# Kernel optimization log

Hardware: AMD Instinct MI355X
Metric: run time of the kernel (lower is better)

Reference implementation:

```python
import jax, jax.numpy as jnp
import numpy as np

N = 50000      # nodes
E = 800000     # edges (avg degree 16)
IN = 128       # in_feats
H = 4          # num_heads
D = 32         # out_feats per head
EF = 32        # edge_feats
NT = 4         # num node types
ET = 8         # num edge types
NEG_SLOPE = 0.2


def setup_inputs() -> dict:
    key = jax.random.key(0)
    ks = jax.random.split(key, 12)
    feat = jax.random.normal(ks[0], (N, IN), dtype=jnp.float32)
    src = jax.random.randint(ks[1], (E,), 0, N, dtype=jnp.int32)
    dst = jax.random.randint(ks[2], (E,), 0, N, dtype=jnp.int32)
    etype = jax.random.randint(ks[3], (E,), 0, ET, dtype=jnp.int32)
    ntype = jax.random.randint(ks[4], (N,), 0, NT, dtype=jnp.int32)
    # learned parameters (xavier-ish scale)
    W_fc = jax.random.normal(ks[5], (H * D, IN), dtype=jnp.float32) * (2.0 / (IN + H * D)) ** 0.5
    W_e = jax.random.normal(ks[6], (H * EF, EF), dtype=jnp.float32) * (2.0 / (EF + H * EF)) ** 0.5
    edge_emb = jax.random.normal(ks[7], (ET, EF), dtype=jnp.float32) * 0.1
    attn_l = jax.random.normal(ks[8], (NT, H, D), dtype=jnp.float32) * 0.1
    attn_r = jax.random.normal(ks[9], (NT, H, D), dtype=jnp.float32) * 0.1
    attn_e = jax.random.normal(ks[10], (ET, H, EF), dtype=jnp.float32) * 0.1
    return dict(feat=feat, W_fc=W_fc, W_e=W_e, edge_emb=edge_emb,
                attn_l=attn_l, attn_r=attn_r, attn_e=attn_e,
                src=src, dst=dst, etype=etype, ntype=ntype)


def reference(feat, W_fc, W_e, edge_emb, attn_l, attn_r, attn_e, src, dst, etype, ntype):
    n = feat.shape[0]
    # node projection: (N, IN) @ (IN, H*D) -> (N, H, D)
    feat_src = (feat @ W_fc.T).reshape(n, H, D)

    # edge-type embedding: original multiplies the etype id (as float) by edge_emb[etype]
    embed_e = etype.astype(feat.dtype)[:, None] * edge_emb[etype]          # (E, EF)
    embed_e = (embed_e @ W_e.T).reshape(-1, H, EF)                          # (E, H, EF)
    ee = jnp.einsum('ehf,ehf->eh', embed_e, attn_e[etype])                  # (E, H)

    # per-node-type attention scores
    el = jnp.einsum('nhd,nhd->nh', feat_src, attn_l[ntype])                 # (N, H)
    er = jnp.einsum('nhd,nhd->nh', feat_src, attn_r[ntype])                 # (N, H)

    e = el[src] + er[dst] + ee                                              # (E, H)
    e = jnp.where(e > 0, e, NEG_SLOPE * e)                                  # leaky relu

    # edge softmax over incoming edges of each destination node
    m = jax.ops.segment_max(e, dst, num_segments=n)                         # (N, H)
    m = jnp.where(jnp.isfinite(m), m, 0.0)                                  # guard empty segments
    ex = jnp.exp(e - m[dst])
    den = jax.ops.segment_sum(ex, dst, num_segments=n)                      # (N, H)
    a = ex / den[dst]                                                       # (E, H)

    # aggregate: rst[v] = sum_{(u->v)} a * feat_src[u]
    msgs = feat_src[src] * a[:, :, None]                                    # (E, H, D)
    rst = jax.ops.segment_sum(msgs, dst, num_segments=n)                    # (N, H, D)
    return rst, a[:, :, None]
```

## Files before the change

kernel.cpp:

```cpp
#include <hip/hip_runtime.h>
#include <hip/hip_bf16.h>

#define NEG_SLOPE 0.2f

typedef __attribute__((ext_vector_type(4))) float f32x4;
typedef __attribute__((ext_vector_type(8))) short s16x8;

__device__ __forceinline__ short f2bf(float x) {
    __hip_bfloat16 h = __float2bfloat16(x);
    return *reinterpret_cast<short*>(&h);
}

#define PCHUNK 64
__global__ __launch_bounds__(256) void k_proj(const float* __restrict__ feat,
                                              const float* __restrict__ Wfc,
                                              __hip_bfloat16* __restrict__ fsrcb,
                                              const float* __restrict__ attn_l,
                                              const float* __restrict__ attn_r,
                                              const int* __restrict__ ntype,
                                              float* __restrict__ el,
                                              float* __restrict__ er, int n) {
    __shared__ short Wb[128 * 128];
    __shared__ float s_al[512], s_ar[512];
    const int t = threadIdx.x;
    for (int idx = t; idx < 128 * 128; idx += 256) {
        int c = idx >> 7, k = idx & 127;
        Wb[c * 128 + ((((k >> 3) ^ (c & 7)) << 3) | (k & 7))] = f2bf(Wfc[idx]);
    }
    s_al[t] = attn_l[t]; s_al[t + 256] = attn_l[t + 256];
    s_ar[t] = attn_r[t]; s_ar[t + 256] = attn_r[t + 256];
    __syncthreads();

    const int w   = t >> 6;
    const int l   = t & 63;
    const int c16 = l & 15;
    const int g0  = l >> 4;
    const int nchunks = (n + PCHUNK - 1) / PCHUNK;

    for (int chunk = blockIdx.x; chunk < nchunks; chunk += gridDim.x) {
        const int rbase = chunk * PCHUNK + w * 16;
        const float* ap = feat + (size_t)min(rbase + c16, n - 1) * 128;
        s16x8 av[4];
        #pragma unroll
        for (int kq = 0; kq < 4; ++kq) {
            float4 q0 = *(const float4*)(ap + g0 * 8 + kq * 32);
            float4 q1 = *(const float4*)(ap + g0 * 8 + kq * 32 + 4);
            s16x8 a;
            a[0] = f2bf(q0.x); a[1] = f2bf(q0.y); a[2] = f2bf(q0.z); a[3] = f2bf(q0.w);
            a[4] = f2bf(q1.x); a[5] = f2bf(q1.y); a[6] = f2bf(q1.z); a[7] = f2bf(q1.w);
            av[kq] = a;
        }
        f32x4 acc[8];
        #pragma unroll
        for (int f = 0; f < 8; ++f) acc[f] = (f32x4)0.f;
        #pragma unroll
        for (int kq = 0; kq < 4; ++kq) {
            const int g = g0 + kq * 4;
            #pragma unroll
            for (int f = 0; f < 8; ++f) {
                const int c = f * 16 + c16;
                const s16x8 bv = *(const s16x8*)&Wb[c * 128 + ((g ^ (c & 7)) << 3)];
                acc[f] = __builtin_amdgcn_mfma_f32_16x16x32_bf16(av[kq], bv, acc[f], 0, 0, 0);
            }
        }
        #pragma unroll
        for (int reg = 0; reg < 4; ++reg) {
            const int rr = rbase + g0 * 4 + reg;
            const bool ok = rr < n;
            if (ok) {
                #pragma unroll
                for (int f = 0; f < 8; ++f)
                    fsrcb[(size_t)rr * 128 + f * 16 + c16] = __float2bfloat16(acc[f][reg]);
            }
            const int nt = ntype[min(rr, n - 1)];
            const float* alp = s_al + nt * 128;
            const float* arp = s_ar + nt * 128;
            float pe[4], pr[4];
            #pragma unroll
            for (int h = 0; h < 4; ++h) {
                float d0 = acc[2 * h][reg], d1 = acc[2 * h + 1][reg];
                pe[h] = d0 * alp[h * 32 + c16] + d1 * alp[h * 32 + 16 + c16];
                pr[h] = d0 * arp[h * 32 + c16] + d1 * arp[h * 32 + 16 + c16];
            }
            #pragma unroll
            for (int msk = 1; msk < 16; msk <<= 1) {
                #pragma unroll
                for (int h = 0; h < 4; ++h) {
                    pe[h] += __shfl_xor(pe[h], msk, 64);
                    pr[h] += __shfl_xor(pr[h], msk, 64);
                }
            }
            if (c16 == 0 && ok) {
                float4 e4; e4.x = pe[0]; e4.y = pe[1]; e4.z = pe[2]; e4.w = pe[3];
                float4 r4; r4.x = pr[0]; r4.y = pr[1]; r4.z = pr[2]; r4.w = pr[3];
                *(float4*)(el + (size_t)rr * 4) = e4;
                *(float4*)(er + (size_t)rr * 4) = r4;
            }
        }
    }
}

__global__ void k_ee(const float* __restrict__ W_e, const float* __restrict__ edge_emb,
                     const float* __restrict__ attn_e, float* __restrict__ eet) {
    int t = threadIdx.x;
    if (t >= 8 * 4) return;
    int et = t >> 2, h = t & 3;
    float ee = 0.f;
    for (int f = 0; f < 32; ++f) {
        float acc = 0.f;
        for (int g = 0; g < 32; ++g)
            acc += W_e[((size_t)h * 32 + f) * 32 + g] * edge_emb[et * 32 + g];
        ee += acc * attn_e[((size_t)et * 4 + h) * 32 + f];
    }
    eet[t] = ee * (float)et;
}

__global__ void k_deg(const int* __restrict__ dst, int* __restrict__ deg, int ne) {
    int e = blockIdx.x * blockDim.x + threadIdx.x;
    if (e < ne) atomicAdd(deg + dst[e], 1);
}

#define SC_ELEMS 1024
__global__ __launch_bounds__(256) void k_scan_sum(const int* __restrict__ deg,
                                                  int* __restrict__ bsum, int n) {
    __shared__ int red[256];
    const int t = threadIdx.x;
    const int base = blockIdx.x * SC_ELEMS;
    int s = 0;
    #pragma unroll
    for (int i = 0; i < 4; ++i) {
        int idx = base + t * 4 + i;
        if (idx < n) s += deg[idx];
    }
    red[t] = s;
    __syncthreads();
    for (int off = 128; off > 0; off >>= 1) {
        if (t < off) red[t] += red[t + off];
        __syncthreads();
    }
    if (t == 0) bsum[blockIdx.x] = red[0];
}

__global__ __launch_bounds__(1024) void k_scan_mid(int* __restrict__ bsum, int nb) {
    __shared__ int sh[1024];
    const int t = threadIdx.x;
    int v = (t < nb) ? bsum[t] : 0;
    sh[t] = v;
    __syncthreads();
    for (int off = 1; off < 1024; off <<= 1) {
        int add = (t >= off) ? sh[t - off] : 0;
        __syncthreads();
        sh[t] += add;
        __syncthreads();
    }
    if (t < nb) bsum[t] = sh[t] - v;
}

__global__ __launch_bounds__(256) void k_scan_out(const int* __restrict__ deg,
                                                  const int* __restrict__ bsum,
                                                  int* __restrict__ offs,
                                                  int* __restrict__ cursor, int n) {
    __shared__ int sh[256];
    const int t = threadIdx.x;
    const int base = blockIdx.x * SC_ELEMS + t * 4;
    int v[4], s = 0;
    #pragma unroll
    for (int i = 0; i < 4; ++i) {
        int idx = base + i;
        v[i] = (idx < n) ? deg[idx] : 0;
        s += v[i];
    }
    sh[t] = s;
    __syncthreads();
    const int mine = s;
    for (int off = 1; off < 256; off <<= 1) {
        int add = (t >= off) ? sh[t - off] : 0;
        __syncthreads();
        sh[t] += add;
        __syncthreads();
    }
    int run = bsum[blockIdx.x] + sh[t] - mine;
    #pragma unroll
    for (int i = 0; i < 4; ++i) {
        int idx = base + i;
        if (idx < n) { offs[idx] = run; cursor[idx] = run; run += v[i]; }
    }
    if (blockIdx.x == gridDim.x - 1 && t == 255) offs[n] = run;
}

__global__ void k_edge(const int* __restrict__ src, const int* __restrict__ dst,
                       const int* __restrict__ etype, const float* __restrict__ el,
                       const float* __restrict__ er, const float* __restrict__ eet,
                       int* __restrict__ cursor, float* __restrict__ pay, int ne) {
    int e = blockIdx.x * blockDim.x + threadIdx.x;
    if (e >= ne) return;
    int s = src[e], d = dst[e], et = etype[e];
    float4 l = *(const float4*)(el + (size_t)s * 4);
    float4 r = *(const float4*)(er + (size_t)d * 4);
    float4 te = *(const float4*)(eet + (size_t)et * 4);
    float4 v;
    v.x = l.x + r.x + te.x;
    v.y = l.y + r.y + te.y;
    v.z = l.z + r.z + te.z;
    v.w = l.w + r.w + te.w;
    v.x = v.x > 0.f ? v.x : NEG_SLOPE * v.x;
    v.y = v.y > 0.f ? v.y : NEG_SLOPE * v.y;
    v.z = v.z > 0.f ? v.z : NEG_SLOPE * v.z;
    v.w = v.w > 0.f ? v.w : NEG_SLOPE * v.w;
    int pos = atomicAdd(cursor + d, 1);
    *(float4*)(pay + (size_t)pos * 8) = v;
    int2 es; es.x = e; es.y = s;
    *(int2*)(pay + (size_t)pos * 8 + 4) = es;
}

#define CHUNK 128
__global__ __launch_bounds__(128) void k_aggfull(const int* __restrict__ offs,
                                                 const float* __restrict__ pay,
                                                 const __hip_bfloat16* __restrict__ fsrcb,
                                                 float* __restrict__ aBuf,
                                                 float* __restrict__ rst) {
    __shared__ int   s_src[CHUNK];
    __shared__ int   s_eid[CHUNK];
    __shared__ float s_sc[4][CHUNK];
    __shared__ float s_p[4][CHUNK];
    __shared__ float s_mr[8];
    const int d = blockIdx.x;
    const int j = threadIdx.x;
    const int h = j >> 5;
    const int b = offs[d], e1 = offs[d + 1];
    const int deg = e1 - b;

    float m = -1e30f, den = 0.f, acc = 0.f;
    for (int c0 = 0; c0 < deg; c0 += CHUNK) {
        const int cn = min(CHUNK, deg - c0);
        if (j < cn) {
            const float* p8 = pay + (size_t)(b + c0 + j) * 8;
            float4 v = *(const float4*)p8;
            int2 es = *(const int2*)(p8 + 4);
            s_sc[0][j] = v.x; s_sc[1][j] = v.y; s_sc[2][j] = v.z; s_sc[3][j] = v.w;
            s_eid[j] = es.x; s_src[j] = es.y;
        }
        __syncthreads();
        float mc = -1e30f;
        for (int k = j & 31; k < cn; k += 32) mc = fmaxf(mc, s_sc[h][k]);
        #pragma unroll
        for (int w = 1; w < 32; w <<= 1) mc = fmaxf(mc, __shfl_xor(mc, w, 64));
        mc = fmaxf(mc, m);
        float scale = __expf(m - mc);
        den *= scale; acc *= scale; m = mc;
        if ((j & 31) == 0) s_mr[h] = m;
        __syncthreads();
        if (j < cn) {
            s_p[0][j] = __expf(s_sc[0][j] - s_mr[0]);
            s_p[1][j] = __expf(s_sc[1][j] - s_mr[1]);
            s_p[2][j] = __expf(s_sc[2][j] - s_mr[2]);
            s_p[3][j] = __expf(s_sc[3][j] - s_mr[3]);
        }
        __syncthreads();
        float dc = 0.f;
        for (int k = j & 31; k < cn; k += 32) dc += s_p[h][k];
        #pragma unroll
        for (int w = 1; w < 32; w <<= 1) dc += __shfl_xor(dc, w, 64);
        den += dc;
        #pragma unroll 4
        for (int k = 0; k < cn; ++k) {
            acc = fmaf(s_p[h][k],
                       __bfloat162float(fsrcb[(size_t)s_src[k] * 128 + j]), acc);
        }
        __syncthreads();
    }
    float rden = (den > 0.f) ? 1.f / den : 0.f;
    rst[(size_t)d * 128 + j] = acc * rden;

    if ((j & 31) == 0) s_mr[4 + h] = rden;
    __syncthreads();

    if (deg <= CHUNK) {
        if (j < deg) {
            float4 a;
            a.x = s_p[0][j] * s_mr[4];
            a.y = s_p[1][j] * s_mr[5];
            a.z = s_p[2][j] * s_mr[6];
            a.w = s_p[3][j] * s_mr[7];
            *(float4*)(aBuf + (size_t)s_eid[j] * 4) = a;
        }
    } else {
        for (int k0 = 0; k0 < deg; k0 += CHUNK) {
            int k = k0 + j;
            if (k < deg) {
                const float* p8 = pay + (size_t)(b + k) * 8;
                float4 v = *(const float4*)p8;
                int e = *(const int*)(p8 + 4);
                float4 a;
                a.x = __expf(v.x - s_mr[0]) * s_mr[4];
                a.y = __expf(v.y - s_mr[1]) * s_mr[5];
                a.z = __expf(v.z - s_mr[2]) * s_mr[6];
                a.w = __expf(v.w - s_mr[3]) * s_mr[7];
                *(float4*)(aBuf + (size_t)e * 4) = a;
            }
        }
    }
}

extern "C" void kernel_launch(void* const* d_in, const int* in_sizes, int n_in,
                              void* d_out, int out_size, void* d_ws, size_t ws_size,
                              hipStream_t stream) {
    const float* feat     = (const float*)d_in[0];
    const float* W_fc     = (const float*)d_in[1];
    const float* W_e      = (const float*)d_in[2];
    const float* edge_emb = (const float*)d_in[3];
    const float* attn_l   = (const float*)d_in[4];
    const float* attn_r   = (const float*)d_in[5];
    const float* attn_e   = (const float*)d_in[6];
    const int* src   = (const int*)d_in[7];
    const int* dst   = (const int*)d_in[8];
    const int* etype = (const int*)d_in[9];
    const int* ntype = (const int*)d_in[10];
    const int n  = in_sizes[0] / 128;
    const int ne = in_sizes[7];

    __hip_bfloat16* fsrcb = (__hip_bfloat16*)d_ws;
    float* pay  = (float*)(fsrcb + (size_t)n * 128);
    float* el   = pay + (size_t)ne * 8;
    float* er   = el + (size_t)n * 4;
    float* eet  = er + (size_t)n * 4;
    int* deg    = (int*)(eet + 32);
    int* offs   = deg + n;
    int* cursor = offs + n + 1;
    int* bsum   = cursor + n;

    float* rst  = (float*)d_out;
    float* aBuf = rst + (size_t)n * 128;

    const int nb = (n + SC_ELEMS - 1) / SC_ELEMS;

    hipMemsetAsync(deg, 0, (size_t)n * sizeof(int), stream);

    k_proj<<<512, 256, 0, stream>>>(feat, W_fc, fsrcb, attn_l, attn_r, ntype, el, er, n);
    k_ee<<<1, 32, 0, stream>>>(W_e, edge_emb, attn_e, eet);
    k_deg<<<(ne + 255) / 256, 256, 0, stream>>>(dst, deg, ne);
    k_scan_sum<<<nb, 256, 0, stream>>>(deg, bsum, n);
    k_scan_mid<<<1, 1024, 0, stream>>>(bsum, nb);
    k_scan_out<<<nb, 256, 0, stream>>>(deg, bsum, offs, cursor, n);
    k_edge<<<(ne + 255) / 256, 256, 0, stream>>>(src, dst, etype, el, er, eet, cursor, pay, ne);
    k_aggfull<<<n, 128, 0, stream>>>(offs, pay, fsrcb, aBuf, rst);
}
```

Baseline: 272.0 us.

## Move edge score computation into aggregation, compact payload, vectorize bf16 gather

Edge scores are no longer computed in the scatter kernel. That kernel now writes an 8-byte payload of packed edge id plus etype and the source id, instead of 32 bytes, which cuts scatter write and aggregation read traffic. The aggregation kernel recomputes leaky-relu scores from el, er and a shared-memory copy of eet. It also gathers two bf16 features per lane, with the two waves splitting edges and reducing through shared memory. The etype table computation is folded into the degree kernel to remove a launch. The change assumes edge ids fit in 24 bits and adds a random el load per edge inside the aggregation kernel.

Measured after the change: 290.6 us. 1.07x slower.

```diff
diff --git a/kernel.cpp b/kernel.cpp
--- a/kernel.cpp
+++ b/kernel.cpp
@@ -100,22 +100,21 @@
     }
 }
 
-__global__ void k_ee(const float* __restrict__ W_e, const float* __restrict__ edge_emb,
-                     const float* __restrict__ attn_e, float* __restrict__ eet) {
-    int t = threadIdx.x;
-    if (t >= 8 * 4) return;
-    int et = t >> 2, h = t & 3;
-    float ee = 0.f;
-    for (int f = 0; f < 32; ++f) {
-        float acc = 0.f;
-        for (int g = 0; g < 32; ++g)
-            acc += W_e[((size_t)h * 32 + f) * 32 + g] * edge_emb[et * 32 + g];
-        ee += acc * attn_e[((size_t)et * 4 + h) * 32 + f];
-    }
-    eet[t] = ee * (float)et;
-}
-
-__global__ void k_deg(const int* __restrict__ dst, int* __restrict__ deg, int ne) {
+__global__ void k_deg(const int* __restrict__ dst, int* __restrict__ deg, int ne,
+                      const float* __restrict__ W_e, const float* __restrict__ edge_emb,
+                      const float* __restrict__ attn_e, float* __restrict__ eet) {
+    if (blockIdx.x == 0 && threadIdx.x < 32) {
+        int t = threadIdx.x;
+        int et = t >> 2, h = t & 3;
+        float ee = 0.f;
+        for (int f = 0; f < 32; ++f) {
+            float acc = 0.f;
+            for (int g = 0; g < 32; ++g)
+                acc += W_e[((size_t)h * 32 + f) * 32 + g] * edge_emb[et * 32 + g];
+            ee += acc * attn_e[((size_t)et * 4 + h) * 32 + f];
+        }
+        eet[t] = ee * (float)et;
+    }
     int e = blockIdx.x * blockDim.x + threadIdx.x;
     if (e < ne) atomicAdd(deg + dst[e], 1);
 }
@@ -189,66 +188,73 @@
 }
 
 __global__ void k_edge(const int* __restrict__ src, const int* __restrict__ dst,
-                       const int* __restrict__ etype, const float* __restrict__ el,
-                       const float* __restrict__ er, const float* __restrict__ eet,
-                       int* __restrict__ cursor, float* __restrict__ pay, int ne) {
+                       const int* __restrict__ etype, int* __restrict__ cursor,
+                       int2* __restrict__ pay, int ne) {
     int e = blockIdx.x * blockDim.x + threadIdx.x;
     if (e >= ne) return;
-    int s = src[e], d = dst[e], et = etype[e];
-    float4 l = *(const float4*)(el + (size_t)s * 4);
-    float4 r = *(const float4*)(er + (size_t)d * 4);
-    float4 te = *(const float4*)(eet + (size_t)et * 4);
-    float4 v;
-    v.x = l.x + r.x + te.x;
-    v.y = l.y + r.y + te.y;
-    v.z = l.z + r.z + te.z;
-    v.w = l.w + r.w + te.w;
-    v.x = v.x > 0.f ? v.x : NEG_SLOPE * v.x;
-    v.y = v.y > 0.f ? v.y : NEG_SLOPE * v.y;
-    v.z = v.z > 0.f ? v.z : NEG_SLOPE * v.z;
-    v.w = v.w > 0.f ? v.w : NEG_SLOPE * v.w;
+    int d = dst[e];
     int pos = atomicAdd(cursor + d, 1);
-    *(float4*)(pay + (size_t)pos * 8) = v;
-    int2 es; es.x = e; es.y = s;
-    *(int2*)(pay + (size_t)pos * 8 + 4) = es;
+    int2 p; p.x = e | (etype[e] << 24); p.y = src[e];
+    pay[pos] = p;
 }
 
 #define CHUNK 128
 __global__ __launch_bounds__(128) void k_aggfull(const int* __restrict__ offs,
-                                                 const float* __restrict__ pay,
+                                                 const int2* __restrict__ pay,
+                                                 const float* __restrict__ el,
+                                                 const float* __restrict__ er,
+                                                 const float* __restrict__ eet,
                                                  const __hip_bfloat16* __restrict__ fsrcb,
                                                  float* __restrict__ aBuf,
                                                  float* __restrict__ rst) {
+    __shared__ int   s_eid[CHUNK];
     __shared__ int   s_src[CHUNK];
-    __shared__ int   s_eid[CHUNK];
-    __shared__ float s_sc[4][CHUNK];
-    __shared__ float s_p[4][CHUNK];
+    __shared__ float s_sc[4][CHUNK + 1];
+    __shared__ float s_p[4][CHUNK + 1];
+    __shared__ float s_eet[32];
+    __shared__ float s_red[128];
     __shared__ float s_mr[8];
     const int d = blockIdx.x;
     const int j = threadIdx.x;
-    const int h = j >> 5;
+    const int w = j >> 6;
+    const int l = j & 63;
+    const int l16 = l & 15;
+    const int h2 = l >> 4;
+    if (j < 32) s_eet[j] = eet[j];
     const int b = offs[d], e1 = offs[d + 1];
     const int deg = e1 - b;
-
-    float m = -1e30f, den = 0.f, acc = 0.f;
+    float4 er4 = *(const float4*)(er + (size_t)d * 4);
+    __syncthreads();
+
+    float mOld = -1e30f, den = 0.f, acc0 = 0.f, acc1 = 0.f;
     for (int c0 = 0; c0 < deg; c0 += CHUNK) {
         const int cn = min(CHUNK, deg - c0);
         if (j < cn) {
-            const float* p8 = pay + (size_t)(b + c0 + j) * 8;
-            float4 v = *(const float4*)p8;
-            int2 es = *(const int2*)(p8 + 4);
+            int2 p2 = pay[b + c0 + j];
+            int e = p2.x & 0xFFFFFF, et = p2.x >> 24, s = p2.y;
+            s_eid[j] = e; s_src[j] = s;
+            float4 lv = *(const float4*)(el + (size_t)s * 4);
+            const float* te = s_eet + et * 4;
+            float4 v;
+            v.x = lv.x + er4.x + te[0];
+            v.y = lv.y + er4.y + te[1];
+            v.z = lv.z + er4.z + te[2];
+            v.w = lv.w + er4.w + te[3];
+            v.x = v.x > 0.f ? v.x : NEG_SLOPE * v.x;
+            v.y = v.y > 0.f ? v.y : NEG_SLOPE * v.y;
+            v.z = v.z > 0.f ? v.z : NEG_SLOPE * v.z;
+            v.w = v.w > 0.f ? v.w : NEG_SLOPE * v.w;
             s_sc[0][j] = v.x; s_sc[1][j] = v.y; s_sc[2][j] = v.z; s_sc[3][j] = v.w;
-            s_eid[j] = es.x; s_src[j] = es.y;
-        }
-        __syncthreads();
-        float mc = -1e30f;
-        for (int k = j & 31; k < cn; k += 32) mc = fmaxf(mc, s_sc[h][k]);
-        #pragma unroll
-        for (int w = 1; w < 32; w <<= 1) mc = fmaxf(mc, __shfl_xor(mc, w, 64));
-        mc = fmaxf(mc, m);
-        float scale = __expf(m - mc);
-        den *= scale; acc *= scale; m = mc;
-        if ((j & 31) == 0) s_mr[h] = m;
+        }
+        __syncthreads();
+        float mc = mOld;
+        for (int k = l16; k < cn; k += 16) mc = fmaxf(mc, s_sc[h2][k]);
+        #pragma unroll
+        for (int msk = 1; msk < 16; msk <<= 1) mc = fmaxf(mc, __shfl_xor(mc, msk, 64));
+        float scale = __expf(mOld - mc);
+        den *= scale; acc0 *= scale; acc1 *= scale;
+        if (w == 0 && l16 == 0) s_mr[h2] = mc;
+        mOld = mc;
         __syncthreads();
         if (j < cn) {
             s_p[0][j] = __expf(s_sc[0][j] - s_mr[0]);
@@ -258,22 +264,30 @@
         }
         __syncthreads();
         float dc = 0.f;
-        for (int k = j & 31; k < cn; k += 32) dc += s_p[h][k];
-        #pragma unroll
-        for (int w = 1; w < 32; w <<= 1) dc += __shfl_xor(dc, w, 64);
+        for (int k = l16; k < cn; k += 16) dc += s_p[h2][k];
+        #pragma unroll
+        for (int msk = 1; msk < 16; msk <<= 1) dc += __shfl_xor(dc, msk, 64);
         den += dc;
-        #pragma unroll 4
-        for (int k = 0; k < cn; ++k) {
-            acc = fmaf(s_p[h][k],
-                       __bfloat162float(fsrcb[(size_t)s_src[k] * 128 + j]), acc);
+        for (int k = w; k < cn; k += 2) {
+            unsigned u = *(const unsigned*)(fsrcb + (size_t)s_src[k] * 128 + 2 * l);
+            float lo = __uint_as_float(u << 16);
+            float hi = __uint_as_float(u & 0xFFFF0000u);
+            float p = s_p[h2][k];
+            acc0 = fmaf(p, lo, acc0);
+            acc1 = fmaf(p, hi, acc1);
         }
         __syncthreads();
     }
     float rden = (den > 0.f) ? 1.f / den : 0.f;
-    rst[(size_t)d * 128 + j] = acc * rden;
-
-    if ((j & 31) == 0) s_mr[4 + h] = rden;
-    __syncthreads();
+    if (w == 1) { s_red[2 * l] = acc0; s_red[2 * l + 1] = acc1; }
+    if (w == 0 && l16 == 0) s_mr[4 + h2] = rden;
+    __syncthreads();
+    if (w == 0) {
+        float2 o;
+        o.x = (acc0 + s_red[2 * l]) * rden;
+        o.y = (acc1 + s_red[2 * l + 1]) * rden;
+        *(float2*)(rst + (size_t)d * 128 + 2 * l) = o;
+    }
 
     if (deg <= CHUNK) {
         if (j < deg) {
@@ -288,9 +302,19 @@
         for (int k0 = 0; k0 < deg; k0 += CHUNK) {
             int k = k0 + j;
             if (k < deg) {
-                const float* p8 = pay + (size_t)(b + k) * 8;
-                float4 v = *(const float4*)p8;
-                int e = *(const int*)(p8 + 4);
+                int2 p2 = pay[b + k];
+                int e = p2.x & 0xFFFFFF, et = p2.x >> 24, s = p2.y;
+                float4 lv = *(const float4*)(el + (size_t)s * 4);
+                const float* te = s_eet + et * 4;
+                float4 v;
+                v.x = lv.x + er4.x + te[0];
+                v.y = lv.y + er4.y + te[1];
+                v.z = lv.z + er4.z + te[2];
+                v.w = lv.w + er4.w + te[3];
+                v.x = v.x > 0.f ? v.x : NEG_SLOPE * v.x;
+                v.y = v.y > 0.f ? v.y : NEG_SLOPE * v.y;
+                v.z = v.z > 0.f ? v.z : NEG_SLOPE * v.z;
+                v.w = v.w > 0.f ? v.w : NEG_SLOPE * v.w;
                 float4 a;
                 a.x = __expf(v.x - s_mr[0]) * s_mr[4];
                 a.y = __expf(v.y - s_mr[1]) * s_mr[5];
@@ -320,8 +344,8 @@
     const int ne = in_sizes[7];
 
     __hip_bfloat16* fsrcb = (__hip_bfloat16*)d_ws;
-    float* pay  = (float*)(fsrcb + (size_t)n * 128);
-    float* el   = pay + (size_t)ne * 8;
+    int2* pay   = (int2*)(fsrcb + (size_t)n * 128);
+    float* el   = (float*)(pay + ne);
     float* er   = el + (size_t)n * 4;
     float* eet  = er + (size_t)n * 4;
     int* deg    = (int*)(eet + 32);
@@ -337,11 +361,10 @@
     hipMemsetAsync(deg, 0, (size_t)n * sizeof(int), stream);
 
     k_proj<<<512, 256, 0, stream>>>(feat, W_fc, fsrcb, attn_l, attn_r, ntype, el, er, n);
-    k_ee<<<1, 32, 0, stream>>>(W_e, edge_emb, attn_e, eet);
-    k_deg<<<(ne + 255) / 256, 256, 0, stream>>>(dst, deg, ne);
+    k_deg<<<(ne + 255) / 256, 256, 0, stream>>>(dst, deg, ne, W_e, edge_emb, attn_e, eet);
     k_scan_sum<<<nb, 256, 0, stream>>>(deg, bsum, n);
     k_scan_mid<<<1, 1024, 0, stream>>>(bsum, nb);
     k_scan_out<<<nb, 256, 0, stream>>>(deg, bsum, offs, cursor, n);
-    k_edge<<<(ne + 255) / 256, 256, 0, stream>>>(src, dst, etype, el, er, eet, cursor, pay, ne);
-    k_aggfull<<<n, 128, 0, stream>>>(offs, pay, fsrcb, aBuf, rst);
-}
+    k_edge<<<(ne + 255) / 256, 256, 0, stream>>>(src, dst, etype, cursor, pay, ne);
+    k_aggfull<<<n, 128, 0, stream>>>(offs, pay, el, er, eet, fsrcb, aBuf, rst);
+}
```
